# Optimization experiments

Hardware: AMD Instinct MI355X
Metric: run time of the kernel (lower is better)

The kernel has to match this reference:

```python
import jax, jax.numpy as jnp
import numpy as np

HASHMAPS = [(50, 32, 1.0), (200, 16, 0.5), (400, 8, 0.25), (400, 4, 0.125), (400, 3, 0.05)]
CONCAT = 63  # 32+16+8+4+3
PRIMES = jnp.array([73856093, 19349663, 83492791], dtype=jnp.int32)
# corner order idx = i*4 + j*2 + k, bit 0 -> floor, bit 1 -> ceil (matches torch loop)
BITS = jnp.array([[i, j, k] for i in range(2) for j in range(2) for k in range(2)], dtype=jnp.int32)  # (8,3)


def _encode(pos, table, vsl):
    # pos: (N,3) float32; table: (hsize, D)
    p = pos / vsl
    fl = jnp.floor(p)
    fl_i = fl.astype(jnp.int32)
    ce_i = jnp.ceil(p).astype(jnp.int32)
    sel = jnp.where(BITS[None, :, :] == 0, fl_i[:, None, :], ce_i[:, None, :])  # (N,8,3) int32
    sp = sel * PRIMES  # int32 wraparound, same as torch
    h = jnp.mod((sp[..., 0] ^ sp[..., 1]) ^ sp[..., 2], table.shape[0])  # (N,8), nonneg
    emb = table[h]  # (N,8,D) gather
    r = p - fl  # (N,3) trilinear fractions
    # faithful to original: frac weights the FLOOR-corner group (m1/m2/m3 masks)
    lin1 = r[:, 0:1, None] * emb[:, :4] + (1.0 - r[:, 0:1, None]) * emb[:, 4:]   # (N,4,D)
    lin2 = r[:, 1:2, None] * lin1[:, :2] + (1.0 - r[:, 1:2, None]) * lin1[:, 2:]  # (N,2,D)
    lin3 = r[:, 2:3] * lin2[:, 0] + (1.0 - r[:, 2:3]) * lin2[:, 1]               # (N,D)
    return lin3


def setup_inputs() -> dict:
    key = jax.random.key(0)
    ks = jax.random.split(key, 16)
    N = 262144
    inp = {"x": jax.random.normal(ks[0], (N, 3), dtype=jnp.float32)}
    for lvl, (hsize, dim, _) in enumerate(HASHMAPS):
        inp[f"emb{lvl}"] = jax.random.normal(ks[1 + lvl], (hsize, dim), dtype=jnp.float32)
    s = 1.0 / np.sqrt(CONCAT)
    inp["Wd1"] = jax.random.uniform(ks[6], (CONCAT, CONCAT), jnp.float32, -s, s)
    inp["bd1"] = jax.random.uniform(ks[7], (CONCAT,), jnp.float32, -s, s)
    inp["Wd2"] = jax.random.uniform(ks[8], (CONCAT, 1), jnp.float32, -s, s)
    inp["bd2"] = jax.random.uniform(ks[9], (1,), jnp.float32, -s, s)
    inp["Wc1"] = jax.random.uniform(ks[10], (CONCAT, CONCAT), jnp.float32, -s, s)
    inp["bc1"] = jax.random.uniform(ks[11], (CONCAT,), jnp.float32, -s, s)
    inp["Wc2"] = jax.random.uniform(ks[12], (CONCAT, 3), jnp.float32, -s, s)
    inp["bc2"] = jax.random.uniform(ks[13], (3,), jnp.float32, -s, s)
    return inp


def reference(x, emb0, emb1, emb2, emb3, emb4, Wd1, bd1, Wd2, bd2, Wc1, bc1, Wc2, bc2):
    tables = [emb0, emb1, emb2, emb3, emb4]
    feats = [_encode(x, tables[i], HASHMAPS[i][2]) for i in range(5)]
    f = jnp.concatenate(feats, axis=1)  # (N,63)
    dense = jax.nn.relu(f @ Wd1 + bd1) @ Wd2 + bd2  # (N,1)
    color = jax.nn.relu(f @ Wc1 + bc1) @ Wc2 + bc2  # (N,3)
    return (dense, color)
```

## Files before the change

kernel.cpp:

```cpp
#include <hip/hip_runtime.h>
#include <hip/hip_fp16.h>


#define NPTS 262144
#define BLOCK 512
#define PTS_PER_TILE 128
#define TILES 2
#define PTS_PER_BLOCK (PTS_PER_TILE * TILES)

#define IMG_TAB   0
#define IMG_WTF   32768
#define IMG_BW    49152
#define IMG_BYTES 51200

#define OFF_L0 0
#define OFF_L1 2000
#define OFF_L2 6000
#define OFF_L3 10800
#define OFF_L4 12400
#define TAB_HALFS 16384

typedef _Float16 f16x8 __attribute__((ext_vector_type(8)));
typedef _Float16 f16x4 __attribute__((ext_vector_type(4)));
typedef float f32x4 __attribute__((ext_vector_type(4)));

__device__ __forceinline__ void async_cp16(const void* g, void* l) {
    __builtin_amdgcn_global_load_lds(
        (__attribute__((address_space(1))) unsigned int*)const_cast<void*>(g),
        (__attribute__((address_space(3))) unsigned int*)l, 16, 0, 0);
}

__global__ void prep_kernel(const float* __restrict__ Wd1, const float* __restrict__ bd1,
                            const float* __restrict__ Wd2,
                            const float* __restrict__ Wc1, const float* __restrict__ bc1,
                            const float* __restrict__ Wc2,
                            const float* __restrict__ e0, const float* __restrict__ e1,
                            const float* __restrict__ e2, const float* __restrict__ e3,
                            const float* __restrict__ e4,
                            void* __restrict__ ws) {
    _Float16* tab = (_Float16*)((char*)ws + IMG_TAB);
    _Float16* wtf = (_Float16*)((char*)ws + IMG_WTF);
    float*    bw  = (float*)((char*)ws + IMG_BW);
    const int gtid = blockIdx.x * blockDim.x + threadIdx.x;
    const int gstr = gridDim.x * blockDim.x;

    for (int i = gtid; i < 1024; i += gstr) {
        int nt = i >> 7, rem = i & 127, s = rem >> 6, l = rem & 63;
        int kq = l >> 4, lo = l & 15, col = nt * 16 + lo;
#pragma unroll
        for (int j = 0; j < 8; ++j) {
            int k = s * 32 + kq * 8 + j;
            float v = 0.f;
            if (k < 63) {
                if (col < 63) v = Wd1[k * 63 + col];
                else if (col >= 64 && col < 127) v = Wc1[k * 63 + (col - 64)];
            }
            wtf[i * 8 + j] = (_Float16)v;
        }
    }
    for (int i = gtid; i < 512; i += gstr) {
        float v = 0.f;
        if (i < 128) {
            if (i < 63) v = bd1[i];
            else if (i >= 64 && i < 127) v = bc1[i - 64];
        } else if (i < 192) {
            int t = i - 128; v = (t < 63) ? Wd2[t] : 0.f;
        } else if (i < 448) {
            int t = i - 192, c = t >> 2, j = t & 3;
            v = (c < 63 && j < 3) ? Wc2[c * 3 + j] : 0.f;
        }
        bw[i] = v;
    }
    for (int idx = gtid; idx < 50 * 40; idx += gstr) {
        int r = idx / 40, c = idx - r * 40;
        tab[OFF_L0 + idx] = (c < 32) ? (_Float16)e0[r * 32 + c] : (_Float16)0.f;
    }
    for (int idx = gtid; idx < 200 * 20; idx += gstr) {
        int r = idx / 20, c = idx - r * 20;
        tab[OFF_L1 + idx] = (c < 16) ? (_Float16)e1[r * 16 + c] : (_Float16)0.f;
    }
    for (int idx = gtid; idx < 400 * 12; idx += gstr) {
        int r = idx / 12, c = idx - r * 12;
        tab[OFF_L2 + idx] = (c < 8) ? (_Float16)e2[r * 8 + c] : (_Float16)0.f;
    }
    for (int idx = gtid; idx < 400 * 4; idx += gstr)
        tab[OFF_L3 + idx] = (_Float16)e3[idx];
    for (int idx = gtid; idx < 400 * 4; idx += gstr) {
        int r = idx >> 2, c = idx & 3;
        tab[OFF_L4 + idx] = (c < 3) ? (_Float16)e4[r * 3 + c] : (_Float16)0.f;
    }
    for (int idx = 14000 + gtid; idx < TAB_HALFS; idx += gstr)
        tab[idx] = (_Float16)0.f;
}

__device__ __forceinline__ int pymod(int v, int H, int sh) {
    unsigned vu = (unsigned)v ^ 0x80000000u;
    unsigned q = __umulhi(vu >> sh, 0x51EB851Fu) >> 3;
    int m = (int)(vu - q * (unsigned)H);
    int h = m - 48;
    return h < 0 ? h + H : h;
}

struct Corner {
    int ax0, ax1, ay0, ay1, az0, az1;
    float rx, ry, rz;
};
__device__ __forceinline__ Corner mkcorner(float px, float py, float pz) {
    Corner c;
    float fx = floorf(px), fy = floorf(py), fz = floorf(pz);
    c.rx = px - fx; c.ry = py - fy; c.rz = pz - fz;
    c.ax0 = (int)((unsigned)(int)fx * 73856093u);
    c.ax1 = (int)((unsigned)(int)ceilf(px) * 73856093u);
    c.ay0 = (int)((unsigned)(int)fy * 19349663u);
    c.ay1 = (int)((unsigned)(int)ceilf(py) * 19349663u);
    c.az0 = (int)((unsigned)(int)fz * 83492791u);
    c.az1 = (int)((unsigned)(int)ceilf(pz) * 83492791u);
    return c;
}

#define CXOR(C, cc) ((((cc) & 4) ? C.ax1 : C.ax0) ^ (((cc) & 2) ? C.ay1 : C.ay0) \
                   ^ (((cc) & 1) ? C.az1 : C.az0))
#define CW(C, cc) ((((cc) & 4) ? (1.f - C.rx) : C.rx) * \
                   (((cc) & 2) ? (1.f - C.ry) : C.ry) * \
                   (((cc) & 1) ? (1.f - C.rz) : C.rz))

#define ROR_ADD(v, CTRL) { \
    int _t = __builtin_amdgcn_update_dpp(0, __float_as_int(v), (CTRL), 0xF, 0xF, true); \
    (v) += __int_as_float(_t); }
__device__ __forceinline__ float rowsum16(float v) {
    ROR_ADD(v, 0x121)
    ROR_ADD(v, 0x122)
    ROR_ADD(v, 0x124)
    ROR_ADD(v, 0x128)
    return v;
}

#define TILE_BODY(ca_, cb_, cb1_, hA_, h0_, h1_, wb_)                          \
{                                                                              \
    const int kq8 = kq * 8;                                                    \
    f16x8 va[8];                                                               \
    _Pragma("unroll")                                                          \
    for (int cc = 0; cc < 8; ++cc)                                             \
        va[cc] = *(const f16x8*)(ldsT + OFF_L0 + hA_[cc] * 40 + kq8);          \
    f16x4 ea[8];                                                               \
    _Pragma("unroll")                                                          \
    for (int cc = 0; cc < 8; ++cc)                                             \
        ea[cc] = *(const f16x4*)(ldsT + tb0 + h0_[cc] * st + fo0);             \
    float fA[8] = {0.f, 0.f, 0.f, 0.f, 0.f, 0.f, 0.f, 0.f};                    \
    _Pragma("unroll")                                                          \
    for (int cc = 0; cc < 8; ++cc) {                                           \
        float w = CW(ca_, cc);                                                 \
        _Pragma("unroll")                                                      \
        for (int j = 0; j < 8; ++j)                                            \
            fA[j] = fmaf((float)va[cc][j], w, fA[j]);                          \
    }                                                                          \
    f16x4 eb[8];                                                               \
    _Pragma("unroll")                                                          \
    for (int cc = 0; cc < 8; ++cc)                                             \
        eb[cc] = *(const f16x4*)(ldsT + tb1 + h1_[cc] * st + fo1);             \
    float fB[8] = {0.f, 0.f, 0.f, 0.f, 0.f, 0.f, 0.f, 0.f};                    \
    _Pragma("unroll")                                                          \
    for (int cc = 0; cc < 8; ++cc) {                                           \
        float w = CW(cb_, cc);                                                 \
        fB[0] = fmaf((float)ea[cc][0], w, fB[0]);                              \
        fB[1] = fmaf((float)ea[cc][1], w, fB[1]);                              \
        fB[2] = fmaf((float)ea[cc][2], w, fB[2]);                              \
        fB[3] = fmaf((float)ea[cc][3], w, fB[3]);                              \
    }                                                                          \
    _Pragma("unroll")                                                          \
    for (int cc = 0; cc < 8; ++cc) {                                           \
        float w = CW(cb1_, cc);                                                \
        fB[4] = fmaf((float)eb[cc][0], w, fB[4]);                              \
        fB[5] = fmaf((float)eb[cc][1], w, fB[5]);                              \
        fB[6] = fmaf((float)eb[cc][2], w, fB[6]);                              \
        fB[7] = fmaf((float)eb[cc][3], w, fB[7]);                              \
    }                                                                          \
    if (q3) fB[7] = 0.f;                                                       \
    union AF { unsigned u[4]; f16x8 h; } a0, a1;                               \
    _Pragma("unroll")                                                          \
    for (int j = 0; j < 4; ++j) {                                              \
        __half2 t0 = __floats2half2_rn(fA[2 * j], fA[2 * j + 1]);              \
        __half2 t1 = __floats2half2_rn(fB[2 * j], fB[2 * j + 1]);              \
        a0.u[j] = *(unsigned*)&t0;                                             \
        a1.u[j] = *(unsigned*)&t1;                                             \
    }                                                                          \
    float pd[4]  = {0.f, 0.f, 0.f, 0.f};                                       \
    float pc0[4] = {0.f, 0.f, 0.f, 0.f};                                       \
    float pc1[4] = {0.f, 0.f, 0.f, 0.f};                                       \
    float pc2[4] = {0.f, 0.f, 0.f, 0.f};                                       \
    _Pragma("unroll")                                                          \
    for (int nt = 0; nt < 8; ++nt) {                                           \
        f16x8 b0 = wtf[(nt * 2 + 0) * 64 + l];                                 \
        f16x8 b1 = wtf[(nt * 2 + 1) * 64 + l];                                 \
        f32x4 c = {0.f, 0.f, 0.f, 0.f};                                        \
        c = __builtin_amdgcn_mfma_f32_16x16x32_f16(a0.h, b0, c, 0, 0, 0);      \
        c = __builtin_amdgcn_mfma_f32_16x16x32_f16(a1.h, b1, c, 0, 0, 0);      \
        float bias = b1c[nt * 16 + lo];                                        \
        if (nt < 4) {                                                          \
            float w2 = w2d[nt * 16 + lo];                                      \
            _Pragma("unroll")                                                  \
            for (int r = 0; r < 4; ++r)                                        \
                pd[r] = fmaf(fmaxf(c[r] + bias, 0.f), w2, pd[r]);              \
        } else {                                                               \
            float4 wc = w2c[(nt - 4) * 16 + lo];                               \
            _Pragma("unroll")                                                  \
            for (int r = 0; r < 4; ++r) {                                      \
                float t = fmaxf(c[r] + bias, 0.f);                             \
                pc0[r] = fmaf(t, wc.x, pc0[r]);                                \
                pc1[r] = fmaf(t, wc.y, pc1[r]);                                \
                pc2[r] = fmaf(t, wc.z, pc2[r]);                                \
            }                                                                  \
        }                                                                      \
    }                                                                          \
    _Pragma("unroll")                                                          \
    for (int r = 0; r < 4; ++r) {                                              \
        pd[r]  = rowsum16(pd[r]);                                              \
        pc0[r] = rowsum16(pc0[r]);                                             \
        pc1[r] = rowsum16(pc1[r]);                                             \
        pc2[r] = rowsum16(pc2[r]);                                             \
    }                                                                          \
    if (lo < 4) {                                                              \
        float badd = (lo == 0) ? bd2v                                          \
                   : ((lo == 1) ? bcx : ((lo == 2) ? bcy : bcz));              \
        _Pragma("unroll")                                                      \
        for (int r = 0; r < 4; ++r) {                                          \
            int row = wb_ + kq * 4 + r;                                        \
            int addr = (lo == 0) ? row : (NPTS + row * 3 + (lo - 1));          \
            float v = (lo == 0) ? pd[r]                                        \
                    : ((lo == 1) ? pc0[r] : ((lo == 2) ? pc1[r] : pc2[r]));    \
            out[addr] = v + badd;                                              \
        }                                                                      \
    }                                                                          \
}

__global__ __launch_bounds__(BLOCK, 6) void nerf_fwd(
    const float* __restrict__ x,
    const float* __restrict__ bd2, const float* __restrict__ bc2,
    const void* __restrict__ ws,
    float* __restrict__ out)
{
    __shared__ __align__(16) char ldsb[IMG_BYTES];
    const int tid = threadIdx.x;

    {
        const char* gsrc = (const char*)ws + tid * 16;
        char* ldst = ldsb + tid * 16;
#pragma unroll
        for (int i = 0; i < 6; ++i)
            async_cp16(gsrc + i * 8192, ldst + i * 8192);
        if (tid < 128)
            async_cp16(gsrc + 6 * 8192, ldst + 6 * 8192);
    }

    const int l  = tid & 63;
    const int lo = l & 15;
    const int kq = l >> 4;
    const int wb0 = blockIdx.x * PTS_PER_BLOCK + (tid >> 6) * 16;
    const int wb1 = wb0 + PTS_PER_TILE;

    const int p0 = wb0 + lo, p1 = wb1 + lo;
    const float x00 = x[3 * p0 + 0], x01 = x[3 * p0 + 1], x02 = x[3 * p0 + 2];
    const float x10 = x[3 * p1 + 0], x11 = x[3 * p1 + 1], x12 = x[3 * p1 + 2];

    const bool q2 = (kq == 2), q3 = (kq == 3);
    const int  g  = kq >> 1;
    const int  H  = 200 << g;
    const int  sh = 3 + g;
    const float sA = q3 ? 8.f : (q2 ? 4.f : 2.f);
    const int tb0 = q3 ? OFF_L3 : (q2 ? OFF_L2 : OFF_L1);
    const int st  = q3 ? 4 : (q2 ? 12 : 20);
    const int fo0 = (kq == 1) ? 8 : 0;
    const int tb1 = q3 ? OFF_L4 : tb0;
    const int fo1 = q3 ? 0 : fo0 + 4;

    Corner ca0 = mkcorner(x00, x01, x02);
    Corner cb0 = mkcorner(x00 * sA, x01 * sA, x02 * sA);
    Corner cc0;
    {
        const float dx = x00 / 0.05f, dy = x01 / 0.05f, dz = x02 / 0.05f;
        const float b1x = q3 ? dx : x00 * sA, b1y = q3 ? dy : x01 * sA,
                    b1z = q3 ? dz : x02 * sA;
        cc0 = mkcorner(b1x, b1y, b1z);
    }
    int hA0[8], h00[8], h10[8];
#pragma unroll
    for (int cc = 0; cc < 8; ++cc) hA0[cc] = pymod(CXOR(ca0, cc), 50, 1);
#pragma unroll
    for (int cc = 0; cc < 8; ++cc) h00[cc] = pymod(CXOR(cb0, cc), H, sh);
#pragma unroll
    for (int cc = 0; cc < 8; ++cc) h10[cc] = pymod(CXOR(cc0, cc), H, sh);

    const float bd2v = bd2[0];
    const float bcx = bc2[0], bcy = bc2[1], bcz = bc2[2];

    __syncthreads();

    const _Float16* ldsT = (const _Float16*)ldsb;
    const f16x8* wtf = (const f16x8*)(ldsb + IMG_WTF);
    const float* b1c = (const float*)(ldsb + IMG_BW);
    const float* w2d = b1c + 128;
    const float4* w2c = (const float4*)(b1c + 192);

    TILE_BODY(ca0, cb0, cc0, hA0, h00, h10, wb0)

    Corner ca1 = mkcorner(x10, x11, x12);
    Corner cb1 = mkcorner(x10 * sA, x11 * sA, x12 * sA);
    Corner cc1;
    {
        const float dx = x10 / 0.05f, dy = x11 / 0.05f, dz = x12 / 0.05f;
        const float b1x = q3 ? dx : x10 * sA, b1y = q3 ? dy : x11 * sA,
                    b1z = q3 ? dz : x12 * sA;
        cc1 = mkcorner(b1x, b1y, b1z);
    }
    int hA1[8], h01[8], h11[8];
#pragma unroll
    for (int cc = 0; cc < 8; ++cc) hA1[cc] = pymod(CXOR(ca1, cc), 50, 1);
#pragma unroll
    for (int cc = 0; cc < 8; ++cc) h01[cc] = pymod(CXOR(cb1, cc), H, sh);
#pragma unroll
    for (int cc = 0; cc < 8; ++cc) h11[cc] = pymod(CXOR(cc1, cc), H, sh);

    TILE_BODY(ca1, cb1, cc1, hA1, h01, h11, wb1)
}

extern "C" void kernel_launch(void* const* d_in, const int* in_sizes, int n_in,
                              void* d_out, int out_size, void* d_ws, size_t ws_size,
                              hipStream_t stream) {
    const float* x   = (const float*)d_in[0];
    const float* e0  = (const float*)d_in[1];
    const float* e1  = (const float*)d_in[2];
    const float* e2  = (const float*)d_in[3];
    const float* e3  = (const float*)d_in[4];
    const float* e4  = (const float*)d_in[5];
    const float* Wd1 = (const float*)d_in[6];
    const float* bd1 = (const float*)d_in[7];
    const float* Wd2 = (const float*)d_in[8];
    const float* bd2 = (const float*)d_in[9];
    const float* Wc1 = (const float*)d_in[10];
    const float* bc1 = (const float*)d_in[11];
    const float* Wc2 = (const float*)d_in[12];
    const float* bc2 = (const float*)d_in[13];
    float* out = (float*)d_out;

    prep_kernel<<<64, 256, 0, stream>>>(Wd1, bd1, Wd2, Wc1, bc1, Wc2,
                                        e0, e1, e2, e3, e4, d_ws);
    nerf_fwd<<<dim3(NPTS / PTS_PER_BLOCK), dim3(BLOCK), 0, stream>>>(
        x, bd2, bc2, d_ws, out);
}
```

Before: 36.13 us.

## Share MLP weight loads across both point tiles and pack bias/W2 into float4

Splits the per-tile body into a hash-encoding frontend and a shared MLP stage, so both tiles' A-fragments are built first and each weight fragment loaded from LDS feeds four MFMAs instead of two. The bias and second-layer weights are repacked in the prep kernel into one float4 per column, replacing three separate LDS loads with one. This roughly doubles the live accumulators and fragments, so launch bounds drop from 6 to 5 waves to leave register headroom, at some cost in occupancy.

```diff
diff --git a/kernel.cpp b/kernel.cpp
--- a/kernel.cpp
+++ b/kernel.cpp
@@ -5,8 +5,7 @@
 #define NPTS 262144
 #define BLOCK 512
 #define PTS_PER_TILE 128
-#define TILES 2
-#define PTS_PER_BLOCK (PTS_PER_TILE * TILES)
+#define PTS_PER_BLOCK 256
 
 #define IMG_TAB   0
 #define IMG_WTF   32768
@@ -23,6 +22,8 @@
 typedef _Float16 f16x8 __attribute__((ext_vector_type(8)));
 typedef _Float16 f16x4 __attribute__((ext_vector_type(4)));
 typedef float f32x4 __attribute__((ext_vector_type(4)));
+
+union AF { unsigned u[4]; f16x8 h; };
 
 __device__ __forceinline__ void async_cp16(const void* g, void* l) {
     __builtin_amdgcn_global_load_lds(
@@ -59,15 +60,16 @@
         }
     }
     for (int i = gtid; i < 512; i += gstr) {
+        int col = i >> 2, j = i & 3;
         float v = 0.f;
-        if (i < 128) {
-            if (i < 63) v = bd1[i];
-            else if (i >= 64 && i < 127) v = bc1[i - 64];
-        } else if (i < 192) {
-            int t = i - 128; v = (t < 63) ? Wd2[t] : 0.f;
-        } else if (i < 448) {
-            int t = i - 192, c = t >> 2, j = t & 3;
-            v = (c < 63 && j < 3) ? Wc2[c * 3 + j] : 0.f;
+        if (j == 0) {
+            if (col < 63) v = bd1[col];
+            else if (col >= 64 && col < 127) v = bc1[col - 64];
+        } else if (col < 64) {
+            if (j == 1 && col < 63) v = Wd2[col];
+        } else {
+            int c2 = col - 64;
+            if (c2 < 63) v = Wc2[c2 * 3 + (j - 1)];
         }
         bw[i] = v;
     }
@@ -135,21 +137,40 @@
     return v;
 }
 
-#define TILE_BODY(ca_, cb_, cb1_, hA_, h0_, h1_, wb_)                          \
+#define MK_HASHES(CA, CB, CBR, HA, H0, H1, X0, X1, X2)                         \
+    Corner CA = mkcorner((X0), (X1), (X2));                                    \
+    Corner CB = mkcorner((X0) * sA, (X1) * sA, (X2) * sA);                     \
+    Corner CBR;                                                                \
+    {                                                                          \
+        const float dx_ = (X0) / 0.05f, dy_ = (X1) / 0.05f, dz_ = (X2) / 0.05f;\
+        const float b1x_ = q3 ? dx_ : (X0) * sA;                               \
+        const float b1y_ = q3 ? dy_ : (X1) * sA;                               \
+        const float b1z_ = q3 ? dz_ : (X2) * sA;                               \
+        CBR = mkcorner(b1x_, b1y_, b1z_);                                      \
+    }                                                                          \
+    int HA[8], H0[8], H1[8];                                                   \
+    _Pragma("unroll")                                                          \
+    for (int cc = 0; cc < 8; ++cc) HA[cc] = pymod(CXOR(CA, cc), 50, 1);        \
+    _Pragma("unroll")                                                          \
+    for (int cc = 0; cc < 8; ++cc) H0[cc] = pymod(CXOR(CB, cc), H, sh);        \
+    _Pragma("unroll")                                                          \
+    for (int cc = 0; cc < 8; ++cc) H1[cc] = pymod(CXOR(CBR, cc), H, sh);
+
+#define FRONTEND(A0, A1, CA, CB, CBR, HA, H0, H1)                              \
 {                                                                              \
     const int kq8 = kq * 8;                                                    \
     f16x8 va[8];                                                               \
     _Pragma("unroll")                                                          \
     for (int cc = 0; cc < 8; ++cc)                                             \
-        va[cc] = *(const f16x8*)(ldsT + OFF_L0 + hA_[cc] * 40 + kq8);          \
+        va[cc] = *(const f16x8*)(ldsT + OFF_L0 + HA[cc] * 40 + kq8);           \
     f16x4 ea[8];                                                               \
     _Pragma("unroll")                                                          \
     for (int cc = 0; cc < 8; ++cc)                                             \
-        ea[cc] = *(const f16x4*)(ldsT + tb0 + h0_[cc] * st + fo0);             \
+        ea[cc] = *(const f16x4*)(ldsT + tb0 + H0[cc] * st + fo0);              \
     float fA[8] = {0.f, 0.f, 0.f, 0.f, 0.f, 0.f, 0.f, 0.f};                    \
     _Pragma("unroll")                                                          \
     for (int cc = 0; cc < 8; ++cc) {                                           \
-        float w = CW(ca_, cc);                                                 \
+        float w = CW(CA, cc);                                                  \
         _Pragma("unroll")                                                      \
         for (int j = 0; j < 8; ++j)                                            \
             fA[j] = fmaf((float)va[cc][j], w, fA[j]);                          \
@@ -157,11 +178,11 @@
     f16x4 eb[8];                                                               \
     _Pragma("unroll")                                                          \
     for (int cc = 0; cc < 8; ++cc)                                             \
-        eb[cc] = *(const f16x4*)(ldsT + tb1 + h1_[cc] * st + fo1);             \
+        eb[cc] = *(const f16x4*)(ldsT + tb1 + H1[cc] * st + fo1);              \
     float fB[8] = {0.f, 0.f, 0.f, 0.f, 0.f, 0.f, 0.f, 0.f};                    \
     _Pragma("unroll")                                                          \
     for (int cc = 0; cc < 8; ++cc) {                                           \
-        float w = CW(cb_, cc);                                                 \
+        float w = CW(CB, cc);                                                  \
         fB[0] = fmaf((float)ea[cc][0], w, fB[0]);                              \
         fB[1] = fmaf((float)ea[cc][1], w, fB[1]);                              \
         fB[2] = fmaf((float)ea[cc][2], w, fB[2]);                              \
@@ -169,71 +190,42 @@
     }                                                                          \
     _Pragma("unroll")                                                          \
     for (int cc = 0; cc < 8; ++cc) {                                           \
-        float w = CW(cb1_, cc);                                                \
+        float w = CW(CBR, cc);                                                 \
         fB[4] = fmaf((float)eb[cc][0], w, fB[4]);                              \
         fB[5] = fmaf((float)eb[cc][1], w, fB[5]);                              \
         fB[6] = fmaf((float)eb[cc][2], w, fB[6]);                              \
         fB[7] = fmaf((float)eb[cc][3], w, fB[7]);                              \
     }                                                                          \
     if (q3) fB[7] = 0.f;                                                       \
-    union AF { unsigned u[4]; f16x8 h; } a0, a1;                               \
     _Pragma("unroll")                                                          \
     for (int j = 0; j < 4; ++j) {                                              \
         __half2 t0 = __floats2half2_rn(fA[2 * j], fA[2 * j + 1]);              \
         __half2 t1 = __floats2half2_rn(fB[2 * j], fB[2 * j + 1]);              \
-        a0.u[j] = *(unsigned*)&t0;                                             \
-        a1.u[j] = *(unsigned*)&t1;                                             \
-    }                                                                          \
-    float pd[4]  = {0.f, 0.f, 0.f, 0.f};                                       \
-    float pc0[4] = {0.f, 0.f, 0.f, 0.f};                                       \
-    float pc1[4] = {0.f, 0.f, 0.f, 0.f};                                       \
-    float pc2[4] = {0.f, 0.f, 0.f, 0.f};                                       \
-    _Pragma("unroll")                                                          \
-    for (int nt = 0; nt < 8; ++nt) {                                           \
-        f16x8 b0 = wtf[(nt * 2 + 0) * 64 + l];                                 \
-        f16x8 b1 = wtf[(nt * 2 + 1) * 64 + l];                                 \
-        f32x4 c = {0.f, 0.f, 0.f, 0.f};                                        \
-        c = __builtin_amdgcn_mfma_f32_16x16x32_f16(a0.h, b0, c, 0, 0, 0);      \
-        c = __builtin_amdgcn_mfma_f32_16x16x32_f16(a1.h, b1, c, 0, 0, 0);      \
-        float bias = b1c[nt * 16 + lo];                                        \
-        if (nt < 4) {                                                          \
-            float w2 = w2d[nt * 16 + lo];                                      \
-            _Pragma("unroll")                                                  \
-            for (int r = 0; r < 4; ++r)                                        \
-                pd[r] = fmaf(fmaxf(c[r] + bias, 0.f), w2, pd[r]);              \
-        } else {                                                               \
-            float4 wc = w2c[(nt - 4) * 16 + lo];                               \
-            _Pragma("unroll")                                                  \
-            for (int r = 0; r < 4; ++r) {                                      \
-                float t = fmaxf(c[r] + bias, 0.f);                             \
-                pc0[r] = fmaf(t, wc.x, pc0[r]);                                \
-                pc1[r] = fmaf(t, wc.y, pc1[r]);                                \
-                pc2[r] = fmaf(t, wc.z, pc2[r]);                                \
-            }                                                                  \
-        }                                                                      \
-    }                                                                          \
+        A0.u[j] = *(unsigned*)&t0;                                             \
+        A1.u[j] = *(unsigned*)&t1;                                             \
+    }                                                                          \
+}
+
+#define REDUCE_STORE(PD, PX, PY, PZ, WB)                                       \
     _Pragma("unroll")                                                          \
     for (int r = 0; r < 4; ++r) {                                              \
-        pd[r]  = rowsum16(pd[r]);                                              \
-        pc0[r] = rowsum16(pc0[r]);                                             \
-        pc1[r] = rowsum16(pc1[r]);                                             \
-        pc2[r] = rowsum16(pc2[r]);                                             \
+        PD[r] = rowsum16(PD[r]); PX[r] = rowsum16(PX[r]);                      \
+        PY[r] = rowsum16(PY[r]); PZ[r] = rowsum16(PZ[r]);                      \
     }                                                                          \
     if (lo < 4) {                                                              \
         float badd = (lo == 0) ? bd2v                                          \
                    : ((lo == 1) ? bcx : ((lo == 2) ? bcy : bcz));              \
         _Pragma("unroll")                                                      \
         for (int r = 0; r < 4; ++r) {                                          \
-            int row = wb_ + kq * 4 + r;                                        \
+            int row = (WB) + kq * 4 + r;                                       \
             int addr = (lo == 0) ? row : (NPTS + row * 3 + (lo - 1));          \
-            float v = (lo == 0) ? pd[r]                                        \
-                    : ((lo == 1) ? pc0[r] : ((lo == 2) ? pc1[r] : pc2[r]));    \
+            float v = (lo == 0) ? PD[r]                                        \
+                    : ((lo == 1) ? PX[r] : ((lo == 2) ? PY[r] : PZ[r]));       \
             out[addr] = v + badd;                                              \
         }                                                                      \
-    }                                                                          \
-}
-
-__global__ __launch_bounds__(BLOCK, 6) void nerf_fwd(
+    }
+
+__global__ __launch_bounds__(BLOCK, 5) void nerf_fwd(
     const float* __restrict__ x,
     const float* __restrict__ bd2, const float* __restrict__ bc2,
     const void* __restrict__ ws,
@@ -273,22 +265,7 @@
     const int tb1 = q3 ? OFF_L4 : tb0;
     const int fo1 = q3 ? 0 : fo0 + 4;
 
-    Corner ca0 = mkcorner(x00, x01, x02);
-    Corner cb0 = mkcorner(x00 * sA, x01 * sA, x02 * sA);
-    Corner cc0;
-    {
-        const float dx = x00 / 0.05f, dy = x01 / 0.05f, dz = x02 / 0.05f;
-        const float b1x = q3 ? dx : x00 * sA, b1y = q3 ? dy : x01 * sA,
-                    b1z = q3 ? dz : x02 * sA;
-        cc0 = mkcorner(b1x, b1y, b1z);
-    }
-    int hA0[8], h00[8], h10[8];
-#pragma unroll
-    for (int cc = 0; cc < 8; ++cc) hA0[cc] = pymod(CXOR(ca0, cc), 50, 1);
-#pragma unroll
-    for (int cc = 0; cc < 8; ++cc) h00[cc] = pymod(CXOR(cb0, cc), H, sh);
-#pragma unroll
-    for (int cc = 0; cc < 8; ++cc) h10[cc] = pymod(CXOR(cc0, cc), H, sh);
+    MK_HASHES(ca0, cb0, cr0, hA0, h00, h10, x00, x01, x02)
 
     const float bd2v = bd2[0];
     const float bcx = bc2[0], bcy = bc2[1], bcz = bc2[2];
@@ -297,30 +274,52 @@
 
     const _Float16* ldsT = (const _Float16*)ldsb;
     const f16x8* wtf = (const f16x8*)(ldsb + IMG_WTF);
-    const float* b1c = (const float*)(ldsb + IMG_BW);
-    const float* w2d = b1c + 128;
-    const float4* w2c = (const float4*)(b1c + 192);
-
-    TILE_BODY(ca0, cb0, cc0, hA0, h00, h10, wb0)
-
-    Corner ca1 = mkcorner(x10, x11, x12);
-    Corner cb1 = mkcorner(x10 * sA, x11 * sA, x12 * sA);
-    Corner cc1;
-    {
-        const float dx = x10 / 0.05f, dy = x11 / 0.05f, dz = x12 / 0.05f;
-        const float b1x = q3 ? dx : x10 * sA, b1y = q3 ? dy : x11 * sA,
-                    b1z = q3 ? dz : x12 * sA;
-        cc1 = mkcorner(b1x, b1y, b1z);
-    }
-    int hA1[8], h01[8], h11[8];
-#pragma unroll
-    for (int cc = 0; cc < 8; ++cc) hA1[cc] = pymod(CXOR(ca1, cc), 50, 1);
-#pragma unroll
-    for (int cc = 0; cc < 8; ++cc) h01[cc] = pymod(CXOR(cb1, cc), H, sh);
-#pragma unroll
-    for (int cc = 0; cc < 8; ++cc) h11[cc] = pymod(CXOR(cc1, cc), H, sh);
-
-    TILE_BODY(ca1, cb1, cc1, hA1, h01, h11, wb1)
+    const float4* wz = (const float4*)(ldsb + IMG_BW);
+
+    AF a0A, a1A;
+    FRONTEND(a0A, a1A, ca0, cb0, cr0, hA0, h00, h10)
+
+    MK_HASHES(ca1, cb1, cr1, hA1, h01, h11, x10, x11, x12)
+    AF a0B, a1B;
+    FRONTEND(a0B, a1B, ca1, cb1, cr1, hA1, h01, h11)
+
+    float pd0[4]  = {0.f, 0.f, 0.f, 0.f}, pd1[4]  = {0.f, 0.f, 0.f, 0.f};
+    float px0[4]  = {0.f, 0.f, 0.f, 0.f}, px1[4]  = {0.f, 0.f, 0.f, 0.f};
+    float py0[4]  = {0.f, 0.f, 0.f, 0.f}, py1[4]  = {0.f, 0.f, 0.f, 0.f};
+    float pz0[4]  = {0.f, 0.f, 0.f, 0.f}, pz1[4]  = {0.f, 0.f, 0.f, 0.f};
+
+#pragma unroll
+    for (int nt = 0; nt < 8; ++nt) {
+        f16x8 b0 = wtf[(nt * 2 + 0) * 64 + l];
+        f16x8 b1 = wtf[(nt * 2 + 1) * 64 + l];
+        f32x4 c0 = {0.f, 0.f, 0.f, 0.f};
+        f32x4 c1 = {0.f, 0.f, 0.f, 0.f};
+        c0 = __builtin_amdgcn_mfma_f32_16x16x32_f16(a0A.h, b0, c0, 0, 0, 0);
+        c0 = __builtin_amdgcn_mfma_f32_16x16x32_f16(a1A.h, b1, c0, 0, 0, 0);
+        c1 = __builtin_amdgcn_mfma_f32_16x16x32_f16(a0B.h, b0, c1, 0, 0, 0);
+        c1 = __builtin_amdgcn_mfma_f32_16x16x32_f16(a1B.h, b1, c1, 0, 0, 0);
+        float4 z = wz[nt * 16 + lo];
+        if (nt < 4) {
+#pragma unroll
+            for (int r = 0; r < 4; ++r) {
+                pd0[r] = fmaf(fmaxf(c0[r] + z.x, 0.f), z.y, pd0[r]);
+                pd1[r] = fmaf(fmaxf(c1[r] + z.x, 0.f), z.y, pd1[r]);
+            }
+        } else {
+#pragma unroll
+            for (int r = 0; r < 4; ++r) {
+                float t0 = fmaxf(c0[r] + z.x, 0.f);
+                float t1 = fmaxf(c1[r] + z.x, 0.f);
+                px0[r] = fmaf(t0, z.y, px0[r]); py0[r] = fmaf(t0, z.z, py0[r]);
+                pz0[r] = fmaf(t0, z.w, pz0[r]);
+                px1[r] = fmaf(t1, z.y, px1[r]); py1[r] = fmaf(t1, z.z, py1[r]);
+                pz1[r] = fmaf(t1, z.w, pz1[r]);
+            }
+        }
+    }
+
+    REDUCE_STORE(pd0, px0, py0, pz0, wb0)
+    REDUCE_STORE(pd1, px1, py1, pz1, wb1)
 }
 
 extern "C" void kernel_launch(void* const* d_in, const int* in_sizes, int n_in,
```

After: 36.02 us. No clear change (-0.3%).
